# Optimization experiments

Hardware: AMD Instinct MI355X
Metric: run time of the kernel (lower is better)

## Reference

```python
import jax, jax.numpy as jnp
import numpy as np

N = 50000      # nodes
E = 800000     # edges (before self-loops)
F_IN = 128     # num_features
HID = 32       # hidden_channels
HEADS = 4
CLS = 40       # num_classes
NEG_SLOPE = 0.2


def setup_inputs() -> dict:
    key = jax.random.key(0)
    ks = jax.random.split(key, 10)
    s = 0.1
    x = jax.random.normal(ks[0], (N, F_IN), jnp.float32)
    edge_index = jax.random.randint(ks[1], (2, E), 0, N, jnp.int32)
    W1 = jax.random.normal(ks[2], (F_IN, HEADS * HID), jnp.float32) * s
    att_src1 = jax.random.normal(ks[3], (HEADS, HID), jnp.float32) * s
    att_dst1 = jax.random.normal(ks[4], (HEADS, HID), jnp.float32) * s
    b1 = jnp.zeros((HEADS * HID,), jnp.float32)
    W2 = jax.random.normal(ks[5], (HEADS * HID, CLS), jnp.float32) * s
    att_src2 = jax.random.normal(ks[6], (1, CLS), jnp.float32) * s
    att_dst2 = jax.random.normal(ks[7], (1, CLS), jnp.float32) * s
    b2 = jnp.zeros((CLS,), jnp.float32)
    return {"x": x, "edge_index": edge_index,
            "W1": W1, "att_src1": att_src1, "att_dst1": att_dst1, "b1": b1,
            "W2": W2, "att_src2": att_src2, "att_dst2": att_dst2, "b2": b2}


def gat_layer(x, src, dst, W, a_src, a_dst, b, concat):
    """PyG GATConv: per-head linear, edge attention logits a_src.h_j + a_dst.h_i,
    LeakyReLU, segment softmax over incoming edges per dst, weighted scatter-sum."""
    n = x.shape[0]
    H, C = a_src.shape
    h = (x @ W).reshape(n, H, C)                       # [N, H, C]
    al_s = jnp.einsum('nhc,hc->nh', h, a_src)          # [N, H]
    al_d = jnp.einsum('nhc,hc->nh', h, a_dst)          # [N, H]
    e = jax.nn.leaky_relu(al_s[src] + al_d[dst], NEG_SLOPE)  # [E, H]
    e_max = jax.lax.stop_gradient(jax.ops.segment_max(e, dst, num_segments=n))
    e = jnp.exp(e - e_max[dst])
    denom = jax.ops.segment_sum(e, dst, num_segments=n)      # [N, H]
    alpha = e / (denom[dst] + 1e-16)                         # [E, H]
    out = jax.ops.segment_sum(h[src] * alpha[:, :, None], dst, num_segments=n)  # [N, H, C]
    out = out.reshape(n, H * C) if concat else out.mean(axis=1)
    return out + b


def reference(x, edge_index, W1, att_src1, att_dst1, b1, W2, att_src2, att_dst2, b2):
    n = x.shape[0]
    loops = jnp.arange(n, dtype=edge_index.dtype)
    src = jnp.concatenate([edge_index[0], loops])  # PyG adds self-loops by default
    dst = jnp.concatenate([edge_index[1], loops])
    h = gat_layer(x, src, dst, W1, att_src1, att_dst1, b1, concat=True)
    h = jax.nn.relu(h)  # dropout is identity in eval mode
    h = gat_layer(h, src, dst, W2, att_src2, att_dst2, b2, concat=False)
    return jax.nn.log_softmax(h, axis=1)
```

## Files before the change

### kernel.cpp

```cpp
#include <hip/hip_runtime.h>
#include <hip/hip_bf16.h>
#include <cstdint>
#include <cstddef>

#define NN 50000
#define EE 800000
#define FIN 128
#define D1 128
#define HEADS 4
#define HID 32
#define CLS 40
#define NEG 0.2f
#define MAXDEG 64
#define BGB 632

typedef __attribute__((ext_vector_type(8))) short short8;
typedef __attribute__((ext_vector_type(4))) float float4v;

union U16 { uint4 u; short8 s; };

__device__ __forceinline__ float bf2f(unsigned short u) {
    union { unsigned int i; float f; } v; v.i = ((unsigned int)u) << 16; return v.f;
}
__device__ __forceinline__ unsigned short f2bf(float f) {
    union { unsigned int i; float f; } v; v.f = f;
    unsigned int r = v.i + 0x7fffu + ((v.i >> 16) & 1u);
    return (unsigned short)(r >> 16);
}

__global__ __launch_bounds__(256, 4) void bg_k(const int* __restrict__ eidx,
                                               int* __restrict__ cnt,
                                               unsigned short* __restrict__ ssrcp,
                                               const float* __restrict__ X,
                                               const float* __restrict__ W,
                                               const float* __restrict__ as1,
                                               const float* __restrict__ ad1,
                                               unsigned int* __restrict__ H1b,
                                               float* __restrict__ ALS1,
                                               float* __restrict__ ALD1) {
    __shared__ uint4 Wl[2048];
    __shared__ float sas[128], sad[128];
    int t = threadIdx.x;

    if (blockIdx.x < BGB) {
        const int4* src4 = (const int4*)eidx;
        const int4* dst4 = (const int4*)(eidx + EE);
        int stride = BGB * 256;
        for (int i4 = blockIdx.x * 256 + t; i4 < EE / 4; i4 += stride) {
            int4 d = dst4[i4];
            int4 s = src4[i4];
            int s0 = atomicAdd(&cnt[d.x], 1);
            int s1 = atomicAdd(&cnt[d.y], 1);
            int s2 = atomicAdd(&cnt[d.z], 1);
            int s3 = atomicAdd(&cnt[d.w], 1);
            if (s0 < MAXDEG - 1) ssrcp[(size_t)d.x * MAXDEG + s0] = (unsigned short)s.x;
            if (s1 < MAXDEG - 1) ssrcp[(size_t)d.y * MAXDEG + s1] = (unsigned short)s.y;
            if (s2 < MAXDEG - 1) ssrcp[(size_t)d.z * MAXDEG + s2] = (unsigned short)s.z;
            if (s3 < MAXDEG - 1) ssrcp[(size_t)d.w * MAXDEG + s3] = (unsigned short)s.w;
        }
        return;
    }

    int bI = blockIdx.x - BGB;
    if (t < 128) { sas[t] = as1[t]; sad[t] = ad1[t]; }
    for (int g = t; g < 2048; g += 256) {
        int ct = g >> 8, rem = g & 255, kc = rem >> 6, l = rem & 63;
        int c = ct * 16 + (l & 15);
        int k0 = kc * 32 + (l >> 4) * 8;
        U16 u;
#pragma unroll
        for (int j = 0; j < 8; j++) u.s[j] = (short)f2bf(W[(k0 + j) * D1 + c]);
        Wl[g] = u.u;
    }
    __syncthreads();

    int wid = t >> 6, lane = t & 63, quad = lane >> 4, lrow = lane & 15;
    int wrow0 = bI * 128 + wid * 32;

    short8 afr[2][4];
#pragma unroll
    for (int rt = 0; rt < 2; rt++) {
        int r = wrow0 + rt * 16 + lrow;
#pragma unroll
        for (int kc = 0; kc < 4; kc++) {
            short8 a = {0, 0, 0, 0, 0, 0, 0, 0};
            if (r < NN) {
                const float* xp = X + (size_t)r * FIN + kc * 32 + quad * 8;
                float4 x0 = *(const float4*)xp;
                float4 x1 = *(const float4*)(xp + 4);
                a[0] = (short)f2bf(x0.x); a[1] = (short)f2bf(x0.y);
                a[2] = (short)f2bf(x0.z); a[3] = (short)f2bf(x0.w);
                a[4] = (short)f2bf(x1.x); a[5] = (short)f2bf(x1.y);
                a[6] = (short)f2bf(x1.z); a[7] = (short)f2bf(x1.w);
            }
            afr[rt][kc] = a;
        }
    }

    float4v acc[2][4];

    for (int cp = 0; cp < 2; ++cp) {
#pragma unroll
        for (int rt = 0; rt < 2; rt++)
#pragma unroll
            for (int c4 = 0; c4 < 4; c4++) acc[rt][c4] = (float4v)(0.f);

#pragma unroll
        for (int c4 = 0; c4 < 4; c4++) {
#pragma unroll
            for (int kc = 0; kc < 4; kc++) {
                U16 b; b.u = Wl[((cp * 4 + c4) * 4 + kc) * 64 + lane];
                acc[0][c4] = __builtin_amdgcn_mfma_f32_16x16x32_bf16(afr[0][kc], b.s, acc[0][c4], 0, 0, 0);
                acc[1][c4] = __builtin_amdgcn_mfma_f32_16x16x32_bf16(afr[1][kc], b.s, acc[1][c4], 0, 0, 0);
            }
        }

#pragma unroll
        for (int rt = 0; rt < 2; rt++) {
#pragma unroll
            for (int reg = 0; reg < 4; reg++) {
                float ps[2] = {0.f, 0.f};
                float pd[2] = {0.f, 0.f};
#pragma unroll
                for (int c4 = 0; c4 < 4; c4++) {
                    float v = acc[rt][c4][reg];
                    int ct = cp * 4 + c4;
                    ps[c4 >> 1] += v * sas[ct * 16 + lrow];
                    pd[c4 >> 1] += v * sad[ct * 16 + lrow];
                }
#pragma unroll
                for (int o = 1; o < 16; o <<= 1) {
#pragma unroll
                    for (int h = 0; h < 2; h++) {
                        ps[h] += __shfl_xor(ps[h], o);
                        pd[h] += __shfl_xor(pd[h], o);
                    }
                }
                int r = wrow0 + rt * 16 + quad * 4 + reg;
                if (lrow == 0 && r < NN) {
                    *(float2*)&ALS1[(size_t)r * 4 + cp * 2] = make_float2(ps[0], ps[1]);
                    *(float2*)&ALD1[(size_t)r * 4 + cp * 2] = make_float2(pd[0], pd[1]);
                }
            }
        }

#pragma unroll
        for (int rt = 0; rt < 2; rt++)
#pragma unroll
            for (int c4 = 0; c4 < 4; c4++)
#pragma unroll
                for (int reg = 0; reg < 4; reg++) {
                    float v = acc[rt][c4][reg];
                    float o = __shfl_xor(v, 1);
                    int r = wrow0 + rt * 16 + quad * 4 + reg;
                    if (((lane & 1) == 0) && r < NN) {
                        unsigned int u = (unsigned int)f2bf(v) | ((unsigned int)f2bf(o) << 16);
                        H1b[(size_t)r * 64 + (cp * 4 + c4) * 8 + (lrow >> 1)] = u;
                    }
                }
    }
}

__global__ __launch_bounds__(256) void gather1_k(const int* __restrict__ cnt,
                                                 const unsigned short* __restrict__ ssrcp,
                                                 const uint4* __restrict__ H1b4,
                                                 const float4* __restrict__ ALS,
                                                 const float4* __restrict__ ALD,
                                                 const float* __restrict__ b1,
                                                 uint4* __restrict__ OUT1b4) {
    __shared__ float wlds[4][MAXDEG][4];
    __shared__ int sidlds[4][MAXDEG];
    int wid = threadIdx.x >> 6, lane = threadIdx.x & 63;
    int v = blockIdx.x * 4 + wid;
    int degE = min(cnt[v], MAXDEG - 1);
    int degT = degE + 1;
    float4 ad = ALD[v];
    float w0 = 0.f, w1 = 0.f, w2 = 0.f, w3 = 0.f;
    if (lane < degT) {
        int s = (lane < degE) ? (int)ssrcp[(size_t)v * MAXDEG + lane] : v;
        sidlds[wid][lane] = s;
        float4 as = ALS[s];
        float l0 = as.x + ad.x; l0 = l0 > 0.f ? l0 : NEG * l0;
        float l1 = as.y + ad.y; l1 = l1 > 0.f ? l1 : NEG * l1;
        float l2 = as.z + ad.z; l2 = l2 > 0.f ? l2 : NEG * l2;
        float l3 = as.w + ad.w; l3 = l3 > 0.f ? l3 : NEG * l3;
        w0 = __expf(l0); w1 = __expf(l1); w2 = __expf(l2); w3 = __expf(l3);
        wlds[wid][lane][0] = w0; wlds[wid][lane][1] = w1;
        wlds[wid][lane][2] = w2; wlds[wid][lane][3] = w3;
    }
    float d0 = w0, d1 = w1, d2 = w2, d3 = w3;
#pragma unroll
    for (int o = 1; o < 64; o <<= 1) {
        d0 += __shfl_xor(d0, o); d1 += __shfl_xor(d1, o);
        d2 += __shfl_xor(d2, o); d3 += __shfl_xor(d3, o);
    }
    __syncthreads();
    int g = lane >> 4, l = lane & 15, head = l >> 2;
    float a0=0.f,a1=0.f,a2=0.f,a3=0.f,a4=0.f,a5=0.f,a6=0.f,a7=0.f;
    {
        int j0 = g, j1 = g + 4, j2 = g + 8, j3 = g + 12;
        uint4 q0 = make_uint4(0,0,0,0), q1 = q0, q2 = q0, q3 = q0;
        float p0 = 0.f, p1 = 0.f, p2 = 0.f, p3 = 0.f;
        if (j0 < degT) { p0 = wlds[wid][j0][head]; q0 = H1b4[(size_t)sidlds[wid][j0] * 16 + l]; }
        if (j1 < degT) { p1 = wlds[wid][j1][head]; q1 = H1b4[(size_t)sidlds[wid][j1] * 16 + l]; }
        if (j2 < degT) { p2 = wlds[wid][j2][head]; q2 = H1b4[(size_t)sidlds[wid][j2] * 16 + l]; }
        if (j3 < degT) { p3 = wlds[wid][j3][head]; q3 = H1b4[(size_t)sidlds[wid][j3] * 16 + l]; }
        for (;;) {
#define ACC8(Q, P)                                           \
            a0 += (P) * bf2f((unsigned short)((Q).x & 0xffffu)); \
            a1 += (P) * bf2f((unsigned short)((Q).x >> 16));     \
            a2 += (P) * bf2f((unsigned short)((Q).y & 0xffffu)); \
            a3 += (P) * bf2f((unsigned short)((Q).y >> 16));     \
            a4 += (P) * bf2f((unsigned short)((Q).z & 0xffffu)); \
            a5 += (P) * bf2f((unsigned short)((Q).z >> 16));     \
            a6 += (P) * bf2f((unsigned short)((Q).w & 0xffffu)); \
            a7 += (P) * bf2f((unsigned short)((Q).w >> 16));
            ACC8(q0, p0) ACC8(q1, p1) ACC8(q2, p2) ACC8(q3, p3)
#undef ACC8
            j0 += 16;
            if (j0 >= degT) break;
            j1 += 16; j2 += 16; j3 += 16;
            p0 = 0.f; p1 = 0.f; p2 = 0.f; p3 = 0.f;
            { p0 = wlds[wid][j0][head]; q0 = H1b4[(size_t)sidlds[wid][j0] * 16 + l]; }
            if (j1 < degT) { p1 = wlds[wid][j1][head]; q1 = H1b4[(size_t)sidlds[wid][j1] * 16 + l]; }
            if (j2 < degT) { p2 = wlds[wid][j2][head]; q2 = H1b4[(size_t)sidlds[wid][j2] * 16 + l]; }
            if (j3 < degT) { p3 = wlds[wid][j3][head]; q3 = H1b4[(size_t)sidlds[wid][j3] * 16 + l]; }
        }
    }
#pragma unroll
    for (int o = 16; o < 64; o <<= 1) {
        a0 += __shfl_xor(a0, o); a1 += __shfl_xor(a1, o);
        a2 += __shfl_xor(a2, o); a3 += __shfl_xor(a3, o);
        a4 += __shfl_xor(a4, o); a5 += __shfl_xor(a5, o);
        a6 += __shfl_xor(a6, o); a7 += __shfl_xor(a7, o);
    }
    if (lane < 16) {
        float den = (head == 0) ? d0 : (head == 1) ? d1 : (head == 2) ? d2 : d3;
        den += 1e-16f;
        float4 bA = *(const float4*)&b1[8 * l];
        float4 bB = *(const float4*)&b1[8 * l + 4];
        float o0 = fmaxf(a0 / den + bA.x, 0.f);
        float o1 = fmaxf(a1 / den + bA.y, 0.f);
        float o2 = fmaxf(a2 / den + bA.z, 0.f);
        float o3 = fmaxf(a3 / den + bA.w, 0.f);
        float o4 = fmaxf(a4 / den + bB.x, 0.f);
        float o5 = fmaxf(a5 / den + bB.y, 0.f);
        float o6 = fmaxf(a6 / den + bB.z, 0.f);
        float o7 = fmaxf(a7 / den + bB.w, 0.f);
        uint4 u;
        u.x = (unsigned int)f2bf(o0) | ((unsigned int)f2bf(o1) << 16);
        u.y = (unsigned int)f2bf(o2) | ((unsigned int)f2bf(o3) << 16);
        u.z = (unsigned int)f2bf(o4) | ((unsigned int)f2bf(o5) << 16);
        u.w = (unsigned int)f2bf(o6) | ((unsigned int)f2bf(o7) << 16);
        OUT1b4[(size_t)v * 16 + l] = u;
    }
}

__global__ __launch_bounds__(256) void gemm2_k(const unsigned int* __restrict__ OUT1b,
                                               const float* __restrict__ W2,
                                               const float* __restrict__ as2,
                                               const float* __restrict__ ad2,
                                               unsigned int* __restrict__ H2b,
                                               float* __restrict__ ALS2,
                                               float* __restrict__ ALD2) {
    __shared__ uint4 Wl[768];
    __shared__ float sas[48], sad[48];
    int t = threadIdx.x;
    if (t < 48) {
        sas[t] = (t < CLS) ? as2[t] : 0.f;
        sad[t] = (t < CLS) ? ad2[t] : 0.f;
    }
    for (int g = t; g < 768; g += 256) {
        int ct = g >> 8, rem = g & 255, kc = rem >> 6, l = rem & 63;
        int c = ct * 16 + (l & 15);
        int k0 = kc * 32 + (l >> 4) * 8;
        U16 u;
#pragma unroll
        for (int j = 0; j < 8; j++)
            u.s[j] = (c < CLS) ? (short)f2bf(W2[(k0 + j) * CLS + c]) : (short)0;
        Wl[g] = u.u;
    }
    __syncthreads();

    int wid = t >> 6, lane = t & 63, quad = lane >> 4, lrow = lane & 15;
    int wrow0 = blockIdx.x * 128 + wid * 32;

    U16 afr[2][4];
#pragma unroll
    for (int rt = 0; rt < 2; rt++) {
        int r = wrow0 + rt * 16 + lrow;
#pragma unroll
        for (int kc = 0; kc < 4; kc++) {
            if (r < NN)
                afr[rt][kc].u = ((const uint4*)OUT1b)[(size_t)r * 16 + kc * 4 + quad];
            else
                afr[rt][kc].u = make_uint4(0, 0, 0, 0);
        }
    }

    float4v acc[2][3];
#pragma unroll
    for (int rt = 0; rt < 2; rt++)
#pragma unroll
        for (int ct = 0; ct < 3; ct++) acc[rt][ct] = (float4v)(0.f);

#pragma unroll
    for (int ct = 0; ct < 3; ct++) {
#pragma unroll
        for (int kc = 0; kc < 4; kc++) {
            U16 b; b.u = Wl[(ct * 4 + kc) * 64 + lane];
            acc[0][ct] = __builtin_amdgcn_mfma_f32_16x16x32_bf16(afr[0][kc].s, b.s, acc[0][ct], 0, 0, 0);
            acc[1][ct] = __builtin_amdgcn_mfma_f32_16x16x32_bf16(afr[1][kc].s, b.s, acc[1][ct], 0, 0, 0);
        }
    }

#pragma unroll
    for (int rt = 0; rt < 2; rt++) {
#pragma unroll
        for (int reg = 0; reg < 4; reg++) {
            float ps = 0.f, pd = 0.f;
#pragma unroll
            for (int ct = 0; ct < 3; ct++) {
                float v = acc[rt][ct][reg];
                ps += v * sas[ct * 16 + lrow];
                pd += v * sad[ct * 16 + lrow];
            }
#pragma unroll
            for (int o = 1; o < 16; o <<= 1) {
                ps += __shfl_xor(ps, o);
                pd += __shfl_xor(pd, o);
            }
            int r = wrow0 + rt * 16 + quad * 4 + reg;
            if (lrow == 0 && r < NN) {
                ALS2[r] = ps;
                ALD2[r] = pd;
            }
        }
    }

#pragma unroll
    for (int rt = 0; rt < 2; rt++)
#pragma unroll
        for (int ct = 0; ct < 3; ct++)
#pragma unroll
            for (int reg = 0; reg < 4; reg++) {
                float v = acc[rt][ct][reg];
                float o = __shfl_xor(v, 1);
                int r = wrow0 + rt * 16 + quad * 4 + reg;
                int c = ct * 16 + lrow;
                if (((lane & 1) == 0) && c < CLS && r < NN) {
                    unsigned int u = (unsigned int)f2bf(v) | ((unsigned int)f2bf(o) << 16);
                    H2b[(size_t)r * 20 + (c >> 1)] = u;
                }
            }
}

__global__ __launch_bounds__(256) void gather2_k(const int* __restrict__ cnt,
                                                 const unsigned short* __restrict__ ssrcp,
                                                 const unsigned int* __restrict__ H2b,
                                                 const float* __restrict__ ALS,
                                                 const float* __restrict__ ALD,
                                                 const float* __restrict__ b2,
                                                 float* __restrict__ out) {
    int wid = threadIdx.x >> 6, t = threadIdx.x & 63;
    int v = blockIdx.x * 4 + wid;
    int degE = min(cnt[v], MAXDEG - 1);
    int degT = degE + 1;
    __shared__ float w[4][MAXDEG];
    __shared__ int sid[4][MAXDEG];
    __shared__ float part[4][3][CLS];
    float den = 0.f;
    float adv = ALD[v];
    if (t < degT) {
        int s = (t < degE) ? (int)ssrcp[(size_t)v * MAXDEG + t] : v;
        sid[wid][t] = s;
        float l = ALS[s] + adv; l = l > 0.f ? l : NEG * l;
        float e = __expf(l);
        w[wid][t] = e; den = e;
    }
    __syncthreads();
    int g = t / 20, c = t % 20;
    if (t < 60) {
        float ax = 0.f, ay = 0.f;
        int j0 = g, j1 = g + 3, j2 = g + 6, j3 = g + 9;
        unsigned int u0 = 0u, u1 = 0u, u2 = 0u, u3 = 0u;
        float p0 = 0.f, p1 = 0.f, p2 = 0.f, p3 = 0.f;
        if (j0 < degT) { p0 = w[wid][j0]; u0 = H2b[(size_t)sid[wid][j0] * 20 + c]; }
        if (j1 < degT) { p1 = w[wid][j1]; u1 = H2b[(size_t)sid[wid][j1] * 20 + c]; }
        if (j2 < degT) { p2 = w[wid][j2]; u2 = H2b[(size_t)sid[wid][j2] * 20 + c]; }
        if (j3 < degT) { p3 = w[wid][j3]; u3 = H2b[(size_t)sid[wid][j3] * 20 + c]; }
        for (;;) {
            ax += p0 * bf2f((unsigned short)(u0 & 0xffffu));
            ay += p0 * bf2f((unsigned short)(u0 >> 16));
            ax += p1 * bf2f((unsigned short)(u1 & 0xffffu));
            ay += p1 * bf2f((unsigned short)(u1 >> 16));
            ax += p2 * bf2f((unsigned short)(u2 & 0xffffu));
            ay += p2 * bf2f((unsigned short)(u2 >> 16));
            ax += p3 * bf2f((unsigned short)(u3 & 0xffffu));
            ay += p3 * bf2f((unsigned short)(u3 >> 16));
            j0 += 12;
            if (j0 >= degT) break;
            j1 += 12; j2 += 12; j3 += 12;
            p0 = 0.f; p1 = 0.f; p2 = 0.f; p3 = 0.f;
            { p0 = w[wid][j0]; u0 = H2b[(size_t)sid[wid][j0] * 20 + c]; }
            if (j1 < degT) { p1 = w[wid][j1]; u1 = H2b[(size_t)sid[wid][j1] * 20 + c]; }
            if (j2 < degT) { p2 = w[wid][j2]; u2 = H2b[(size_t)sid[wid][j2] * 20 + c]; }
            if (j3 < degT) { p3 = w[wid][j3]; u3 = H2b[(size_t)sid[wid][j3] * 20 + c]; }
        }
        part[wid][g][2 * c] = ax;
        part[wid][g][2 * c + 1] = ay;
    }
#pragma unroll
    for (int o = 32; o > 0; o >>= 1) den += __shfl_xor(den, o);
    __syncthreads();
    float z = (t < CLS) ? (part[wid][0][t] + part[wid][1][t] + part[wid][2][t]) / (den + 1e-16f) + b2[t]
                        : -1e30f;
    float mx = z;
#pragma unroll
    for (int o = 32; o > 0; o >>= 1) mx = fmaxf(mx, __shfl_xor(mx, o));
    float ex = (t < CLS) ? __expf(z - mx) : 0.f;
    float se = ex;
#pragma unroll
    for (int o = 32; o > 0; o >>= 1) se += __shfl_xor(se, o);
    if (t < CLS) out[(size_t)v * CLS + t] = z - mx - __logf(se);
}

extern "C" void kernel_launch(void* const* d_in, const int* in_sizes, int n_in,
                              void* d_out, int out_size, void* d_ws, size_t ws_size,
                              hipStream_t stream) {
    const float* x   = (const float*)d_in[0];
    const int*   eix = (const int*)d_in[1];
    const float* W1  = (const float*)d_in[2];
    const float* as1 = (const float*)d_in[3];
    const float* ad1 = (const float*)d_in[4];
    const float* b1  = (const float*)d_in[5];
    const float* W2  = (const float*)d_in[6];
    const float* as2 = (const float*)d_in[7];
    const float* ad2 = (const float*)d_in[8];
    const float* b2  = (const float*)d_in[9];
    float* out = (float*)d_out;

    char* p = (char*)d_ws;
    auto carve = [&](size_t bytes) -> void* {
        void* r = (void*)p;
        p += (bytes + 255) & ~(size_t)255;
        return r;
    };
    unsigned int* H1b   = (unsigned int*)carve((size_t)NN * 64 * 4);
    unsigned int* OUT1b = (unsigned int*)carve((size_t)NN * 64 * 4);
    unsigned int* H2b   = (unsigned int*)carve((size_t)NN * 20 * 4);
    float* ALS1 = (float*)carve((size_t)NN * 4 * 4);
    float* ALD1 = (float*)carve((size_t)NN * 4 * 4);
    float* ALS2 = (float*)carve((size_t)NN * 4);
    float* ALD2 = (float*)carve((size_t)NN * 4);
    int* cnt    = (int*)carve((size_t)NN * 4);
    unsigned short* ssrcp = (unsigned short*)carve((size_t)NN * MAXDEG * 2);

    hipMemsetAsync(cnt, 0, (size_t)NN * 4, stream);

    int gemmBlocks = (NN + 127) / 128;
    bg_k<<<BGB + gemmBlocks, 256, 0, stream>>>(eix, cnt, ssrcp, x, W1, as1, ad1,
                                               H1b, ALS1, ALD1);
    gather1_k<<<NN / 4, 256, 0, stream>>>(cnt, ssrcp, (const uint4*)H1b,
                                          (const float4*)ALS1, (const float4*)ALD1,
                                          b1, (uint4*)OUT1b);
    gemm2_k<<<(NN + 127) / 128, 256, 0, stream>>>(OUT1b, W2, as2, ad2, H2b, ALS2, ALD2);
    gather2_k<<<NN / 4, 256, 0, stream>>>(cnt, ssrcp, H2b, ALS2, ALD2, b2, out);
}
```

Measured before the change: 226.7 us.

## Fuse layer-1 gather with layer-2 projection and pad degree counters

The layer-1 aggregation kernel and the layer-2 MFMA GEMM are merged into one kernel. Each wave now projects its node's 128-wide hidden vector through W2 with a scalar FP32 dot-product loop from LDS, then writes H2 and the layer-2 attention logits directly. This removes the OUT1 intermediate buffer round trip and one kernel launch. In exchange, every 4-node block reloads the full 20 KB W2 into LDS, which raises L2 traffic and LDS pressure, and the MFMA matmul is replaced by scalar FMAs. Separately, the per-node degree counters are padded to 64-byte strides to reduce atomic contention on shared cache lines, at the cost of a larger memset and footprint.

```diff
diff --git a/kernel.cpp b/kernel.cpp
--- a/kernel.cpp
+++ b/kernel.cpp
@@ -12,6 +12,7 @@
 #define CLS 40
 #define NEG 0.2f
 #define MAXDEG 64
+#define CPAD 16
 #define BGB 632
 
 typedef __attribute__((ext_vector_type(8))) short short8;
@@ -49,10 +50,10 @@
         for (int i4 = blockIdx.x * 256 + t; i4 < EE / 4; i4 += stride) {
             int4 d = dst4[i4];
             int4 s = src4[i4];
-            int s0 = atomicAdd(&cnt[d.x], 1);
-            int s1 = atomicAdd(&cnt[d.y], 1);
-            int s2 = atomicAdd(&cnt[d.z], 1);
-            int s3 = atomicAdd(&cnt[d.w], 1);
+            int s0 = atomicAdd(&cnt[(size_t)d.x * CPAD], 1);
+            int s1 = atomicAdd(&cnt[(size_t)d.y * CPAD], 1);
+            int s2 = atomicAdd(&cnt[(size_t)d.z * CPAD], 1);
+            int s3 = atomicAdd(&cnt[(size_t)d.w * CPAD], 1);
             if (s0 < MAXDEG - 1) ssrcp[(size_t)d.x * MAXDEG + s0] = (unsigned short)s.x;
             if (s1 < MAXDEG - 1) ssrcp[(size_t)d.y * MAXDEG + s1] = (unsigned short)s.y;
             if (s2 < MAXDEG - 1) ssrcp[(size_t)d.z * MAXDEG + s2] = (unsigned short)s.z;
@@ -161,18 +162,30 @@
     }
 }
 
-__global__ __launch_bounds__(256) void gather1_k(const int* __restrict__ cnt,
-                                                 const unsigned short* __restrict__ ssrcp,
-                                                 const uint4* __restrict__ H1b4,
-                                                 const float4* __restrict__ ALS,
-                                                 const float4* __restrict__ ALD,
-                                                 const float* __restrict__ b1,
-                                                 uint4* __restrict__ OUT1b4) {
+__global__ __launch_bounds__(256) void g1g2_k(const int* __restrict__ cnt,
+                                              const unsigned short* __restrict__ ssrcp,
+                                              const uint4* __restrict__ H1b4,
+                                              const float4* __restrict__ ALS,
+                                              const float4* __restrict__ ALD,
+                                              const float* __restrict__ b1,
+                                              const float* __restrict__ W2,
+                                              const float* __restrict__ as2,
+                                              const float* __restrict__ ad2,
+                                              unsigned int* __restrict__ H2b,
+                                              float* __restrict__ ALS2,
+                                              float* __restrict__ ALD2) {
     __shared__ float wlds[4][MAXDEG][4];
     __shared__ int sidlds[4][MAXDEG];
-    int wid = threadIdx.x >> 6, lane = threadIdx.x & 63;
+    __shared__ float W2s[FIN * CLS];
+    __shared__ float out1s[4][FIN];
+    __shared__ float sas2s[CLS], sad2s[CLS];
+    int tid = threadIdx.x;
+    if (tid < CLS) { sas2s[tid] = as2[tid]; sad2s[tid] = ad2[tid]; }
+    for (int i = tid; i < FIN * CLS; i += 256) W2s[i] = W2[i];
+
+    int wid = tid >> 6, lane = tid & 63;
     int v = blockIdx.x * 4 + wid;
-    int degE = min(cnt[v], MAXDEG - 1);
+    int degE = min(cnt[(size_t)v * CPAD], MAXDEG - 1);
     int degT = degE + 1;
     float4 ad = ALD[v];
     float w0 = 0.f, w1 = 0.f, w2 = 0.f, w3 = 0.f;
@@ -206,7 +219,7 @@
         if (j2 < degT) { p2 = wlds[wid][j2][head]; q2 = H1b4[(size_t)sidlds[wid][j2] * 16 + l]; }
         if (j3 < degT) { p3 = wlds[wid][j3][head]; q3 = H1b4[(size_t)sidlds[wid][j3] * 16 + l]; }
         for (;;) {
-#define ACC8(Q, P)                                           \
+#define ACC8(Q, P)                                               \
             a0 += (P) * bf2f((unsigned short)((Q).x & 0xffffu)); \
             a1 += (P) * bf2f((unsigned short)((Q).x >> 16));     \
             a2 += (P) * bf2f((unsigned short)((Q).y & 0xffffu)); \
@@ -239,120 +252,36 @@
         den += 1e-16f;
         float4 bA = *(const float4*)&b1[8 * l];
         float4 bB = *(const float4*)&b1[8 * l + 4];
-        float o0 = fmaxf(a0 / den + bA.x, 0.f);
-        float o1 = fmaxf(a1 / den + bA.y, 0.f);
-        float o2 = fmaxf(a2 / den + bA.z, 0.f);
-        float o3 = fmaxf(a3 / den + bA.w, 0.f);
-        float o4 = fmaxf(a4 / den + bB.x, 0.f);
-        float o5 = fmaxf(a5 / den + bB.y, 0.f);
-        float o6 = fmaxf(a6 / den + bB.z, 0.f);
-        float o7 = fmaxf(a7 / den + bB.w, 0.f);
-        uint4 u;
-        u.x = (unsigned int)f2bf(o0) | ((unsigned int)f2bf(o1) << 16);
-        u.y = (unsigned int)f2bf(o2) | ((unsigned int)f2bf(o3) << 16);
-        u.z = (unsigned int)f2bf(o4) | ((unsigned int)f2bf(o5) << 16);
-        u.w = (unsigned int)f2bf(o6) | ((unsigned int)f2bf(o7) << 16);
-        OUT1b4[(size_t)v * 16 + l] = u;
-    }
-}
-
-__global__ __launch_bounds__(256) void gemm2_k(const unsigned int* __restrict__ OUT1b,
-                                               const float* __restrict__ W2,
-                                               const float* __restrict__ as2,
-                                               const float* __restrict__ ad2,
-                                               unsigned int* __restrict__ H2b,
-                                               float* __restrict__ ALS2,
-                                               float* __restrict__ ALD2) {
-    __shared__ uint4 Wl[768];
-    __shared__ float sas[48], sad[48];
-    int t = threadIdx.x;
-    if (t < 48) {
-        sas[t] = (t < CLS) ? as2[t] : 0.f;
-        sad[t] = (t < CLS) ? ad2[t] : 0.f;
-    }
-    for (int g = t; g < 768; g += 256) {
-        int ct = g >> 8, rem = g & 255, kc = rem >> 6, l = rem & 63;
-        int c = ct * 16 + (l & 15);
-        int k0 = kc * 32 + (l >> 4) * 8;
-        U16 u;
-#pragma unroll
-        for (int j = 0; j < 8; j++)
-            u.s[j] = (c < CLS) ? (short)f2bf(W2[(k0 + j) * CLS + c]) : (short)0;
-        Wl[g] = u.u;
-    }
-    __syncthreads();
-
-    int wid = t >> 6, lane = t & 63, quad = lane >> 4, lrow = lane & 15;
-    int wrow0 = blockIdx.x * 128 + wid * 32;
-
-    U16 afr[2][4];
-#pragma unroll
-    for (int rt = 0; rt < 2; rt++) {
-        int r = wrow0 + rt * 16 + lrow;
-#pragma unroll
-        for (int kc = 0; kc < 4; kc++) {
-            if (r < NN)
-                afr[rt][kc].u = ((const uint4*)OUT1b)[(size_t)r * 16 + kc * 4 + quad];
-            else
-                afr[rt][kc].u = make_uint4(0, 0, 0, 0);
-        }
-    }
-
-    float4v acc[2][3];
-#pragma unroll
-    for (int rt = 0; rt < 2; rt++)
-#pragma unroll
-        for (int ct = 0; ct < 3; ct++) acc[rt][ct] = (float4v)(0.f);
-
-#pragma unroll
-    for (int ct = 0; ct < 3; ct++) {
-#pragma unroll
-        for (int kc = 0; kc < 4; kc++) {
-            U16 b; b.u = Wl[(ct * 4 + kc) * 64 + lane];
-            acc[0][ct] = __builtin_amdgcn_mfma_f32_16x16x32_bf16(afr[0][kc].s, b.s, acc[0][ct], 0, 0, 0);
-            acc[1][ct] = __builtin_amdgcn_mfma_f32_16x16x32_bf16(afr[1][kc].s, b.s, acc[1][ct], 0, 0, 0);
-        }
-    }
-
-#pragma unroll
-    for (int rt = 0; rt < 2; rt++) {
-#pragma unroll
-        for (int reg = 0; reg < 4; reg++) {
-            float ps = 0.f, pd = 0.f;
-#pragma unroll
-            for (int ct = 0; ct < 3; ct++) {
-                float v = acc[rt][ct][reg];
-                ps += v * sas[ct * 16 + lrow];
-                pd += v * sad[ct * 16 + lrow];
-            }
-#pragma unroll
-            for (int o = 1; o < 16; o <<= 1) {
-                ps += __shfl_xor(ps, o);
-                pd += __shfl_xor(pd, o);
-            }
-            int r = wrow0 + rt * 16 + quad * 4 + reg;
-            if (lrow == 0 && r < NN) {
-                ALS2[r] = ps;
-                ALD2[r] = pd;
-            }
-        }
-    }
-
-#pragma unroll
-    for (int rt = 0; rt < 2; rt++)
-#pragma unroll
-        for (int ct = 0; ct < 3; ct++)
-#pragma unroll
-            for (int reg = 0; reg < 4; reg++) {
-                float v = acc[rt][ct][reg];
-                float o = __shfl_xor(v, 1);
-                int r = wrow0 + rt * 16 + quad * 4 + reg;
-                int c = ct * 16 + lrow;
-                if (((lane & 1) == 0) && c < CLS && r < NN) {
-                    unsigned int u = (unsigned int)f2bf(v) | ((unsigned int)f2bf(o) << 16);
-                    H2b[(size_t)r * 20 + (c >> 1)] = u;
-                }
-            }
+        float* op = &out1s[wid][8 * l];
+        op[0] = fmaxf(a0 / den + bA.x, 0.f);
+        op[1] = fmaxf(a1 / den + bA.y, 0.f);
+        op[2] = fmaxf(a2 / den + bA.z, 0.f);
+        op[3] = fmaxf(a3 / den + bA.w, 0.f);
+        op[4] = fmaxf(a4 / den + bB.x, 0.f);
+        op[5] = fmaxf(a5 / den + bB.y, 0.f);
+        op[6] = fmaxf(a6 / den + bB.z, 0.f);
+        op[7] = fmaxf(a7 / den + bB.w, 0.f);
+    }
+    int c = (lane < CLS) ? lane : (CLS - 1);
+    float z = 0.f;
+#pragma unroll 8
+    for (int k = 0; k < FIN; k++) z += out1s[wid][k] * W2s[k * CLS + c];
+    if (lane >= CLS) z = 0.f;
+
+    float ps = (lane < CLS) ? z * sas2s[lane] : 0.f;
+    float pd = (lane < CLS) ? z * sad2s[lane] : 0.f;
+#pragma unroll
+    for (int o = 1; o < 64; o <<= 1) {
+        ps += __shfl_xor(ps, o);
+        pd += __shfl_xor(pd, o);
+    }
+    if (lane == 0) { ALS2[v] = ps; ALD2[v] = pd; }
+
+    float zn = __shfl_down(z, 1);
+    if (lane < CLS && (lane & 1) == 0) {
+        unsigned int u = (unsigned int)f2bf(z) | ((unsigned int)f2bf(zn) << 16);
+        H2b[(size_t)v * 20 + (lane >> 1)] = u;
+    }
 }
 
 __global__ __launch_bounds__(256) void gather2_k(const int* __restrict__ cnt,
@@ -364,7 +293,7 @@
                                                  float* __restrict__ out) {
     int wid = threadIdx.x >> 6, t = threadIdx.x & 63;
     int v = blockIdx.x * 4 + wid;
-    int degE = min(cnt[v], MAXDEG - 1);
+    int degE = min(cnt[(size_t)v * CPAD], MAXDEG - 1);
     int degT = degE + 1;
     __shared__ float w[4][MAXDEG];
     __shared__ int sid[4][MAXDEG];
@@ -447,23 +376,21 @@
         return r;
     };
     unsigned int* H1b   = (unsigned int*)carve((size_t)NN * 64 * 4);
-    unsigned int* OUT1b = (unsigned int*)carve((size_t)NN * 64 * 4);
     unsigned int* H2b   = (unsigned int*)carve((size_t)NN * 20 * 4);
     float* ALS1 = (float*)carve((size_t)NN * 4 * 4);
     float* ALD1 = (float*)carve((size_t)NN * 4 * 4);
     float* ALS2 = (float*)carve((size_t)NN * 4);
     float* ALD2 = (float*)carve((size_t)NN * 4);
-    int* cnt    = (int*)carve((size_t)NN * 4);
+    int* cnt    = (int*)carve((size_t)NN * CPAD * 4);
     unsigned short* ssrcp = (unsigned short*)carve((size_t)NN * MAXDEG * 2);
 
-    hipMemsetAsync(cnt, 0, (size_t)NN * 4, stream);
+    hipMemsetAsync(cnt, 0, (size_t)NN * CPAD * 4, stream);
 
     int gemmBlocks = (NN + 127) / 128;
     bg_k<<<BGB + gemmBlocks, 256, 0, stream>>>(eix, cnt, ssrcp, x, W1, as1, ad1,
                                                H1b, ALS1, ALD1);
-    gather1_k<<<NN / 4, 256, 0, stream>>>(cnt, ssrcp, (const uint4*)H1b,
-                                          (const float4*)ALS1, (const float4*)ALD1,
-                                          b1, (uint4*)OUT1b);
-    gemm2_k<<<(NN + 127) / 128, 256, 0, stream>>>(OUT1b, W2, as2, ad2, H2b, ALS2, ALD2);
+    g1g2_k<<<NN / 4, 256, 0, stream>>>(cnt, ssrcp, (const uint4*)H1b,
+                                       (const float4*)ALS1, (const float4*)ALD1,
+                                       b1, W2, as2, ad2, H2b, ALS2, ALD2);
     gather2_k<<<NN / 4, 256, 0, stream>>>(cnt, ssrcp, H2b, ALS2, ALD2, b2, out);
 }
```

Result: slower. 252.7 us (+11.5%).
